# Performance work log

Hardware: AMD Instinct MI355X
Metric: run time of the kernel (lower is better)

Reference implementation:

```python
import jax, jax.numpy as jnp
import numpy as np

H = 800          # config.param.hidden_size (768 bert + 32 pos)
BERT_H = 768
POS_DIM = 32
NHEAD = 8
DH = 100         # gat_nhidden; NHEAD*DH == H
GAT_LAYERS = 2
N_EVENTS = 66
N_ROLES = 122
EPS = 0.1        # label smoothing
NEG_SLOPE = 0.2  # GATConv leaky_relu slope


def bilstm(x, Wih_f, Whh_f, b_f, Wih_b, Whh_b, b_b):
    """x: [B,T,D] -> [B,T,2H] (torch gate order i,f,g,o)."""
    def run(xs, Wih, Whh, b):
        B = xs.shape[1]; Hd = Whh.shape[1]
        def step(carry, xt):
            h, c = carry
            g = xt @ Wih.T + h @ Whh.T + b
            i, f, gg, o = jnp.split(g, 4, axis=-1)
            c = jax.nn.sigmoid(f) * c + jax.nn.sigmoid(i) * jnp.tanh(gg)
            h = jax.nn.sigmoid(o) * jnp.tanh(c)
            return (h, c), h
        init = (jnp.zeros((B, Hd), xs.dtype), jnp.zeros((B, Hd), xs.dtype))
        _, hs = jax.lax.scan(step, init, xs)
        return hs
    xt = jnp.swapaxes(x, 0, 1)                      # [T,B,D]
    hf = run(xt, Wih_f, Whh_f, b_f)
    hb = run(xt[::-1], Wih_b, Whh_b, b_b)[::-1]
    return jnp.swapaxes(jnp.concatenate([hf, hb], -1), 0, 1)


def gat_conv(x, src, dst, W, a_src, a_dst, bias):
    """PyG GATConv, concat heads, with self-loops. x:[n,H], src/dst:[E]."""
    n = x.shape[0]
    loops = jnp.arange(n)
    s = jnp.concatenate([src, loops])
    d = jnp.concatenate([dst, loops])
    h = (x @ W).reshape(n, NHEAD, DH)
    a_s = jnp.einsum('nhd,hd->nh', h, a_src)
    a_d = jnp.einsum('nhd,hd->nh', h, a_dst)
    e = jax.nn.leaky_relu(a_s[s] + a_d[d], NEG_SLOPE)              # [E,nh]
    m = jnp.full((n, NHEAD), -jnp.inf, x.dtype).at[d].max(e)       # segment max
    ex = jnp.exp(e - m[d])
    den = jnp.zeros((n, NHEAD), x.dtype).at[d].add(ex)
    alpha = ex / den[d]
    out = jnp.zeros((n, NHEAD, DH), x.dtype).at[d].add(alpha[..., None] * h[s])
    return out.reshape(n, NHEAD * DH) + bias


def label_smooth_ce(logits, target):
    c = logits.shape[-1]
    logp = jax.nn.log_softmax(logits, axis=-1)
    smooth = -logp.sum(-1)
    nll = -jnp.take_along_axis(logp, target[..., None], axis=-1)[..., 0]
    return smooth * EPS / c + (1.0 - EPS) * nll


def setup_inputs() -> dict:
    key = jax.random.key(0)
    ks = iter(jax.random.split(key, 32))
    B, S, E = 4, 128, 256
    std = 0.02
    inp = {}
    inp['bert_out'] = jax.random.normal(next(ks), (B, S + 1, BERT_H), jnp.float32)
    inp['pos_ids'] = jax.random.randint(next(ks), (B, S), 0, 31)
    inp['edge_src'] = jax.random.randint(next(ks), (B, E), 0, S)
    inp['edge_dst'] = jax.random.randint(next(ks), (B, E), 0, S)
    inp['start_labels'] = jax.random.randint(next(ks), (B, S, S), 0, N_EVENTS)
    inp['end_labels'] = jax.random.randint(next(ks), (B, S, S), 0, N_EVENTS)
    # parameters
    inp['pos_table'] = std * jax.random.normal(next(ks), (31, POS_DIM), jnp.float32)
    for sfx in ('f', 'b'):
        inp[f'Wih_{sfx}'] = std * jax.random.normal(next(ks), (4 * H, H), jnp.float32)
        inp[f'Whh_{sfx}'] = std * jax.random.normal(next(ks), (4 * H, H), jnp.float32)
        inp[f'bl_{sfx}'] = jnp.zeros((4 * H,), jnp.float32)
    inp['lstm_fc_W'] = std * jax.random.normal(next(ks), (2 * H, H), jnp.float32)
    inp['lstm_fc_b'] = jnp.zeros((H,), jnp.float32)
    inp['table_W'] = std * jax.random.normal(next(ks), (2 * H, H), jnp.float32)
    inp['table_b'] = jnp.zeros((H,), jnp.float32)
    inp['gat_W'] = std * jax.random.normal(next(ks), (H, NHEAD * DH), jnp.float32)
    inp['gat_asrc'] = std * jax.random.normal(next(ks), (NHEAD, DH), jnp.float32)
    inp['gat_adst'] = std * jax.random.normal(next(ks), (NHEAD, DH), jnp.float32)
    inp['gat_bias'] = jnp.zeros((NHEAD * DH,), jnp.float32)
    inp['trig_W'] = std * jax.random.normal(next(ks), (H, N_EVENTS), jnp.float32)
    inp['trig_b'] = jnp.zeros((N_EVENTS,), jnp.float32)
    inp['rs_W'] = std * jax.random.normal(next(ks), (H, N_ROLES), jnp.float32)
    inp['rs_b'] = jnp.zeros((N_ROLES,), jnp.float32)
    inp['re_W'] = std * jax.random.normal(next(ks), (H, N_ROLES), jnp.float32)
    inp['re_b'] = jnp.zeros((N_ROLES,), jnp.float32)
    return inp


def reference(bert_out, pos_ids, edge_src, edge_dst, start_labels, end_labels,
              pos_table, Wih_f, Whh_f, bl_f, Wih_b, Whh_b, bl_b,
              lstm_fc_W, lstm_fc_b, table_W, table_b,
              gat_W, gat_asrc, gat_adst, gat_bias,
              trig_W, trig_b, rs_W, rs_b, re_W, re_b):
    B, S = pos_ids.shape
    # POS embedding, prepend zero vector for [CLS] position
    pos_emb = pos_table[pos_ids]                                   # [B,S,32]
    pos_emb = jnp.concatenate(
        [jnp.zeros((B, 1, POS_DIM), bert_out.dtype), pos_emb], axis=1)
    x = jnp.concatenate([bert_out, pos_emb], axis=-1)              # [B,S+1,800]
    lstm_out = bilstm(x, Wih_f, Whh_f, bl_f, Wih_b, Whh_b, bl_b)   # [B,S+1,1600]
    x = x + jax.nn.relu(lstm_out @ lstm_fc_W + lstm_fc_b)
    x = x[:, 1:, :]                                                # drop CLS -> [B,S,800]

    # per-sample residual GAT stack (eval mode: dropout is identity)
    def gat_stack(xi, si, di):
        for _ in range(GAT_LAYERS):
            xi = xi + jax.nn.relu(gat_conv(xi, si, di, gat_W, gat_asrc, gat_adst, gat_bias))
        return xi
    x = jax.vmap(gat_stack)(x, edge_src, edge_dst)                 # [B,S,800]

    # pairwise table: cat(x_i, x_j) -> fc -> gelu
    x1 = jnp.broadcast_to(x[:, :, None, :], (B, S, S, H))
    x2 = jnp.broadcast_to(x[:, None, :, :], (B, S, S, H))
    s_tab = jax.nn.gelu(jnp.concatenate([x1, x2], -1) @ table_W + table_b)  # [B,S,S,800]

    eye = jnp.eye(S, dtype=start_labels.dtype)
    trig_mask = eye                                                # [S,S]
    arg_mask = 1 - eye
    trig_maskf = trig_mask.astype(s_tab.dtype)
    arg_maskf = arg_mask.astype(s_tab.dtype)

    trig_logits = s_tab @ trig_W + trig_b                          # [B,S,S,66]
    arg1_logits = s_tab @ rs_W + rs_b                              # [B,S,S,122]
    arg2_logits = s_tab @ re_W + re_b

    def masked_mean(loss, maskf):
        return (loss * maskf).sum((1, 2)) / maskf.sum()

    l1 = masked_mean(label_smooth_ce(trig_logits, start_labels * trig_mask), trig_maskf)
    l2 = masked_mean(label_smooth_ce(arg1_logits, start_labels * arg_mask), arg_maskf)
    l3 = masked_mean(label_smooth_ce(arg2_logits, end_labels * arg_mask), arg_maskf)
    total_loss = (l1 + l2 + l3).sum()

    trig_pred = jnp.argmax(trig_logits, -1)
    a1_pred = jnp.argmax(arg1_logits + jnp.swapaxes(arg1_logits, 1, 2), -1)
    a2_pred = jnp.argmax(arg2_logits + jnp.swapaxes(arg2_logits, 1, 2), -1)
    results1 = trig_pred * trig_mask + a1_pred * arg_mask
    results2 = trig_pred * trig_mask + a2_pred * arg_mask
    return total_loss, results1, results2
```

## Files before the change

kernel.cpp:

```cpp
#include <hip/hip_runtime.h>
#include <hip/hip_bf16.h>

#define B4 4
#define S128 128
#define T129 129
#define H800 800
#define E256 256
#define NE 66
#define NR 122
#define DPW 8
#define NWGD 100

typedef float f32x4 __attribute__((ext_vector_type(4)));

#define HB_ROW 900

__device__ __forceinline__ float gelu_f(float x) {
    float t = 0.7978845608028654f * (x + 0.044715f * x * x * x);
    float e = __expf(2.f * t);
    float th = 1.f - 2.f / (e + 1.f);
    return 0.5f * x * (1.f + th);
}

__device__ __forceinline__ float embed_at(const float* __restrict__ bert,
                                          const int* __restrict__ pids,
                                          const float* __restrict__ ptab,
                                          int m, int c)
{
    if (c < 768) return bert[(size_t)m * 768 + c];
    int t = m % T129, b = m / T129;
    if (t == 0) return 0.f;
    return ptab[pids[b * S128 + t - 1] * 32 + (c - 768)];
}

template<int AMODE, int BTRANS, int EPI>
__global__ __launch_bounds__(256) void k_gemm(const float* __restrict__ A, const float* __restrict__ Bm,
                                              const float* __restrict__ bias, const float* __restrict__ res,
                                              float* __restrict__ C, int M, int N, int K)
{
    __shared__ float As[16][68];
    __shared__ float Bs[16][68];
    int m0 = blockIdx.x * 64, n0 = blockIdx.y * 64;
    int tid = threadIdx.x;
    int tm = tid & 15, tn = tid >> 4;
    float acc[4][4] = {};
    for (int k0 = 0; k0 < K; k0 += 16) {
        {
            int kk = tid & 15, mmb = tid >> 4;
            #pragma unroll
            for (int q = 0; q < 4; q++) {
                int mm = mmb + q * 16;
                int m = m0 + mm;
                float v = 0.f;
                if (m < M) {
                    int row = (AMODE == 1) ? (m + (m >> 7) + 1) : m;
                    v = A[(size_t)row * K + k0 + kk];
                }
                As[kk][mm] = v;
            }
        }
        if (BTRANS == 0) {
            int nn = (tid & 15) * 4, kk2 = tid >> 4;
            int n = n0 + nn;
            float t0, t1, t2, t3;
            if (n + 3 < N) {
                const float4 bv = *(const float4*)&Bm[(size_t)(k0 + kk2) * N + n];
                t0 = bv.x; t1 = bv.y; t2 = bv.z; t3 = bv.w;
            } else {
                t0 = (n + 0 < N) ? Bm[(size_t)(k0 + kk2) * N + n + 0] : 0.f;
                t1 = (n + 1 < N) ? Bm[(size_t)(k0 + kk2) * N + n + 1] : 0.f;
                t2 = (n + 2 < N) ? Bm[(size_t)(k0 + kk2) * N + n + 2] : 0.f;
                t3 = (n + 3 < N) ? Bm[(size_t)(k0 + kk2) * N + n + 3] : 0.f;
            }
            Bs[kk2][nn + 0] = t0; Bs[kk2][nn + 1] = t1; Bs[kk2][nn + 2] = t2; Bs[kk2][nn + 3] = t3;
        } else {
            int kk = tid & 15, nnb = tid >> 4;
            #pragma unroll
            for (int q = 0; q < 4; q++) {
                int nn = nnb + q * 16;
                int n = n0 + nn;
                Bs[kk][nn] = (n < N) ? Bm[(size_t)n * K + k0 + kk] : 0.f;
            }
        }
        __syncthreads();
        #pragma unroll
        for (int kk = 0; kk < 16; kk++) {
            float4 a = *(const float4*)&As[kk][tm * 4];
            float4 bb = *(const float4*)&Bs[kk][tn * 4];
            float av[4] = {a.x, a.y, a.z, a.w};
            float bv[4] = {bb.x, bb.y, bb.z, bb.w};
            #pragma unroll
            for (int xx = 0; xx < 4; xx++)
                #pragma unroll
                for (int yy = 0; yy < 4; yy++)
                    acc[xx][yy] += av[xx] * bv[yy];
        }
        __syncthreads();
    }
    #pragma unroll
    for (int xx = 0; xx < 4; xx++) {
        int m = m0 + tm * 4 + xx;
        if (m >= M) continue;
        #pragma unroll
        for (int yy = 0; yy < 4; yy++) {
            int n = n0 + tn * 4 + yy;
            if (n >= N) continue;
            float v = acc[xx][yy];
            if (bias) v += bias[n];
            if (EPI == 1) v = res[(size_t)m * N + n] + fmaxf(v, 0.f);
            C[(size_t)m * N + n] = v;
        }
    }
}

__global__ __launch_bounds__(256) void k_gemm_wih(const float* __restrict__ bert,
                                                  const int* __restrict__ pids,
                                                  const float* __restrict__ ptab,
                                                  const float* __restrict__ Wf, const float* __restrict__ Wb,
                                                  const float* __restrict__ bf, const float* __restrict__ bb_,
                                                  float* __restrict__ C)
{
    __shared__ float As[16][68];
    __shared__ float Bs[16][68];
    const int M = 516, K = 800, N = 6400;
    int m0 = blockIdx.x * 64, n0 = blockIdx.y * 64;
    const float* W  = (n0 < 3200) ? Wf : Wb;
    const float* bi = (n0 < 3200) ? bf : bb_;
    int nb = (n0 < 3200) ? n0 : (n0 - 3200);
    int tid = threadIdx.x;
    int tm = tid & 15, tn = tid >> 4;
    int kk_s = tid & 15, mmb = tid >> 4;
    int mrow[4]; int pofs[4]; bool mok[4];
    #pragma unroll
    for (int q = 0; q < 4; q++) {
        int m = m0 + mmb + q * 16;
        mrow[q] = m;
        mok[q] = m < M;
        int t = m % T129, b = m / T129;
        pofs[q] = (mok[q] && t > 0) ? pids[b * S128 + t - 1] * 32 : -1;
    }
    float acc[4][4] = {};
    for (int k0 = 0; k0 < K; k0 += 16) {
        {
            int c = k0 + kk_s;
            #pragma unroll
            for (int q = 0; q < 4; q++) {
                float v = 0.f;
                if (mok[q]) {
                    if (c < 768) v = bert[(size_t)mrow[q] * 768 + c];
                    else         v = (pofs[q] < 0) ? 0.f : ptab[pofs[q] + c - 768];
                }
                As[kk_s][mmb + q * 16] = v;
            }
        }
        {
            int kk = tid & 15, nnb = tid >> 4;
            #pragma unroll
            for (int q = 0; q < 4; q++) {
                int nn = nnb + q * 16;
                Bs[kk][nn] = W[(size_t)(nb + nn) * K + k0 + kk];
            }
        }
        __syncthreads();
        #pragma unroll
        for (int kk = 0; kk < 16; kk++) {
            float4 a = *(const float4*)&As[kk][tm * 4];
            float4 bb = *(const float4*)&Bs[kk][tn * 4];
            float av[4] = {a.x, a.y, a.z, a.w};
            float bv[4] = {bb.x, bb.y, bb.z, bb.w};
            #pragma unroll
            for (int xx = 0; xx < 4; xx++)
                #pragma unroll
                for (int yy = 0; yy < 4; yy++)
                    acc[xx][yy] += av[xx] * bv[yy];
        }
        __syncthreads();
    }
    #pragma unroll
    for (int xx = 0; xx < 4; xx++) {
        int m = m0 + tm * 4 + xx;
        if (m >= M) continue;
        #pragma unroll
        for (int yy = 0; yy < 4; yy++) {
            int n = n0 + tn * 4 + yy;
            C[(size_t)m * N + n] = acc[xx][yy] + bi[nb + (n - n0)];
        }
    }
}

__global__ __launch_bounds__(256) void k_gemm_fc(const float* __restrict__ A, const float* __restrict__ Bm,
                                                 const float* __restrict__ bias,
                                                 const float* __restrict__ bert, const int* __restrict__ pids,
                                                 const float* __restrict__ ptab, float* __restrict__ C)
{
    __shared__ float As[16][68];
    __shared__ float Bs[16][68];
    const int M = 516, N = 800, K = 1600;
    int m0 = blockIdx.x * 64, n0 = blockIdx.y * 64;
    int tid = threadIdx.x;
    int tm = tid & 15, tn = tid >> 4;
    float acc[4][4] = {};
    for (int k0 = 0; k0 < K; k0 += 16) {
        {
            int kk = tid & 15, mmb = tid >> 4;
            #pragma unroll
            for (int q = 0; q < 4; q++) {
                int mm = mmb + q * 16;
                int m = m0 + mm;
                As[kk][mm] = (m < M) ? A[(size_t)m * K + k0 + kk] : 0.f;
            }
        }
        {
            int nn = (tid & 15) * 4, kk2 = tid >> 4;
            int n = n0 + nn;
            if (n + 3 < N) {
                *(float4*)&Bs[kk2][nn] = *(const float4*)&Bm[(size_t)(k0 + kk2) * N + n];
            } else {
                #pragma unroll
                for (int q = 0; q < 4; q++)
                    Bs[kk2][nn + q] = (n + q < N) ? Bm[(size_t)(k0 + kk2) * N + n + q] : 0.f;
            }
        }
        __syncthreads();
        #pragma unroll
        for (int kk = 0; kk < 16; kk++) {
            float4 a = *(const float4*)&As[kk][tm * 4];
            float4 bb = *(const float4*)&Bs[kk][tn * 4];
            float av[4] = {a.x, a.y, a.z, a.w};
            float bv[4] = {bb.x, bb.y, bb.z, bb.w};
            #pragma unroll
            for (int xx = 0; xx < 4; xx++)
                #pragma unroll
                for (int yy = 0; yy < 4; yy++)
                    acc[xx][yy] += av[xx] * bv[yy];
        }
        __syncthreads();
    }
    #pragma unroll
    for (int xx = 0; xx < 4; xx++) {
        int m = m0 + tm * 4 + xx;
        if (m >= M) continue;
        #pragma unroll
        for (int yy = 0; yy < 4; yy++) {
            int n = n0 + tn * 4 + yy;
            if (n >= N) continue;
            float v = fmaxf(acc[xx][yy] + bias[n], 0.f);
            C[(size_t)m * N + n] = embed_at(bert, pids, ptab, m, n) + v;
        }
    }
}

__global__ __launch_bounds__(256) void k_gemm_uv(const float* __restrict__ A, const float* __restrict__ tW,
                                                 const float* __restrict__ tb, float* __restrict__ C)
{
    __shared__ float As[16][68];
    __shared__ float Bs[16][68];
    const int M = 512, K = 800, N = 1600;
    int m0 = blockIdx.x * 64, n0 = blockIdx.y * 64;
    int tid = threadIdx.x;
    int tm = tid & 15, tn = tid >> 4;
    float acc[4][4] = {};
    for (int k0 = 0; k0 < K; k0 += 16) {
        {
            int kk = tid & 15, mmb = tid >> 4;
            #pragma unroll
            for (int q = 0; q < 4; q++) {
                int mm = mmb + q * 16;
                As[kk][mm] = A[(size_t)(m0 + mm) * K + k0 + kk];
            }
        }
        {
            int nn = (tid & 15) * 4, kk2 = tid >> 4;
            #pragma unroll
            for (int q = 0; q < 4; q++) {
                int n = n0 + nn + q;
                Bs[kk2][nn + q] = (n < 800) ? tW[(size_t)(k0 + kk2) * 800 + n]
                                            : tW[(size_t)(800 + k0 + kk2) * 800 + (n - 800)];
            }
        }
        __syncthreads();
        #pragma unroll
        for (int kk = 0; kk < 16; kk++) {
            float4 a = *(const float4*)&As[kk][tm * 4];
            float4 bb = *(const float4*)&Bs[kk][tn * 4];
            float av[4] = {a.x, a.y, a.z, a.w};
            float bv[4] = {bb.x, bb.y, bb.z, bb.w};
            #pragma unroll
            for (int xx = 0; xx < 4; xx++)
                #pragma unroll
                for (int yy = 0; yy < 4; yy++)
                    acc[xx][yy] += av[xx] * bv[yy];
        }
        __syncthreads();
    }
    #pragma unroll
    for (int xx = 0; xx < 4; xx++) {
        int m = m0 + tm * 4 + xx;
        #pragma unroll
        for (int yy = 0; yy < 4; yy++) {
            int n = n0 + tn * 4 + yy;
            float v = acc[xx][yy];
            if (n < 800) v += tb[n];
            C[(size_t)m * N + n] = v;
        }
    }
}

__global__ __launch_bounds__(256) void k_lstm(const float* __restrict__ xW,
                                              const float* __restrict__ Whhf, const float* __restrict__ Whhb,
                                              float* __restrict__ lstm, float* __restrict__ hpk)
{
    __shared__ float hb[4][HB_ROW];
    __shared__ float gsum[25][32][4];
    __shared__ float gg[128];
    int wg = blockIdx.x;
    int dir = wg >= NWGD ? 1 : 0;
    int wgd = dir ? wg - NWGD : wg;
    const float* Whh = dir ? Whhb : Whhf;
    const float* xWd = xW + dir * 3200;
    int tid = threadIdx.x;
    bool dotth = tid < 200;
    int d = tid & 7, sl = tid >> 3;
    int k0 = sl * 32;
    int rb = tid & 3, rd = (tid >> 2) & 7, rg = tid >> 5;
    int lane = tid & 63;

    float wreg[4][32];
    if (dotth) {
        #pragma unroll
        for (int g = 0; g < 4; g++) {
            const float* wp = Whh + (size_t)(g * 800 + wgd * DPW + d) * 800 + k0;
            #pragma unroll
            for (int q = 0; q < 32; q += 4)
                *(float4*)&wreg[g][q] = *(const float4*)&wp[q];
        }
    }
    for (int i = tid; i < 4 * HB_ROW; i += 256) (&hb[0][0])[i] = 0.f;
    __syncthreads();

    float cst = 0.f;

    for (int step = 0; step < 129; step++) {
        int t = dir ? (128 - step) : step;
        float xq = 0.f;
        if (tid < 128)
            xq = xWd[(size_t)(rb * T129 + t) * 6400 + rg * 800 + wgd * DPW + rd];
        if (step > 0) {
            int tprev = dir ? (t + 1) : (t - 1);
            if (tid < 200) {
                const f32x4* pb = (const f32x4*)(hpk + (size_t)(dir * 129 + tprev) * 3200);
                const f32x4* p0 = pb + tid;
                const f32x4* p1 = pb + tid + 200;
                const f32x4* p2 = pb + tid + 400;
                const f32x4* p3 = pb + tid + 600;
                f32x4 v0, v1, v2, v3;
                long long iters = 0;
                for (;;) {
                    asm volatile(
                        "global_load_dwordx4 %0, %4, off sc0 sc1\n\t"
                        "global_load_dwordx4 %1, %5, off sc0 sc1\n\t"
                        "global_load_dwordx4 %2, %6, off sc0 sc1\n\t"
                        "global_load_dwordx4 %3, %7, off sc0 sc1\n\t"
                        "s_waitcnt vmcnt(0)"
                        : "=&v"(v0), "=&v"(v1), "=&v"(v2), "=&v"(v3)
                        : "v"(p0), "v"(p1), "v"(p2), "v"(p3)
                        : "memory");
                    bool ok = fabsf(v0.x) < 1.5f && fabsf(v0.y) < 1.5f &&
                              fabsf(v0.z) < 1.5f && fabsf(v0.w) < 1.5f &&
                              fabsf(v1.x) < 1.5f && fabsf(v1.y) < 1.5f &&
                              fabsf(v1.z) < 1.5f && fabsf(v1.w) < 1.5f &&
                              fabsf(v2.x) < 1.5f && fabsf(v2.y) < 1.5f &&
                              fabsf(v2.z) < 1.5f && fabsf(v2.w) < 1.5f &&
                              fabsf(v3.x) < 1.5f && fabsf(v3.y) < 1.5f &&
                              fabsf(v3.z) < 1.5f && fabsf(v3.w) < 1.5f;
                    if (ok) break;
                    if (++iters > 20000000LL) break;
                }
                {
                    int s0 = tid;
                    int p_ = (s0 >> 3) * 8 + (s0 & 1) * 4;
                    ((f32x4*)&hb[0][0])[((s0 & 7) >> 1) * 225 + (p_ >> 5) * 9 + ((p_ & 31) >> 2)] = v0;
                }
                {
                    int s1 = tid + 200;
                    int p_ = (s1 >> 3) * 8 + (s1 & 1) * 4;
                    ((f32x4*)&hb[0][0])[((s1 & 7) >> 1) * 225 + (p_ >> 5) * 9 + ((p_ & 31) >> 2)] = v1;
                }
                {
                    int s2 = tid + 400;
                    int p_ = (s2 >> 3) * 8 + (s2 & 1) * 4;
                    ((f32x4*)&hb[0][0])[((s2 & 7) >> 1) * 225 + (p_ >> 5) * 9 + ((p_ & 31) >> 2)] = v2;
                }
                {
                    int s3 = tid + 600;
                    int p_ = (s3 >> 3) * 8 + (s3 & 1) * 4;
                    ((f32x4*)&hb[0][0])[((s3 & 7) >> 1) * 225 + (p_ >> 5) * 9 + ((p_ & 31) >> 2)] = v3;
                }
            }
            __syncthreads();
        }
        if (dotth) {
            float a[4][4] = {};
            #pragma unroll
            for (int b = 0; b < 4; b++) {
                const float* hrow = &hb[b][0];
                #pragma unroll
                for (int q = 0; q < 32; q += 4) {
                    float4 h = *(const float4*)&hrow[sl * 36 + q];
                    #pragma unroll
                    for (int g = 0; g < 4; g++)
                        a[g][b] += wreg[g][q] * h.x + wreg[g][q + 1] * h.y
                                 + wreg[g][q + 2] * h.z + wreg[g][q + 3] * h.w;
                }
            }
            #pragma unroll
            for (int g = 0; g < 4; g++)
                *(float4*)&gsum[sl][g * 8 + d][0] = make_float4(a[g][0], a[g][1], a[g][2], a[g][3]);
        }
        __syncthreads();
        if (tid < 128) {
            float s = xq;
            #pragma unroll
            for (int ss = 0; ss < 25; ss++) s += gsum[ss][rg * 8 + rd][rb];
            gg[tid] = s;
        }
        __syncthreads();
        float hv = 0.f;
        if (tid < 32) {
            int dd = tid & 7, bb2 = tid >> 3;
            float gi = gg[(0 << 5) | (dd << 2) | bb2];
            float gf = gg[(1 << 5) | (dd << 2) | bb2];
            float gG = gg[(2 << 5) | (dd << 2) | bb2];
            float go = gg[(3 << 5) | (dd << 2) | bb2];
            float si = 1.f / (1.f + __expf(-gi));
            float sf = 1.f / (1.f + __expf(-gf));
            float so = 1.f / (1.f + __expf(-go));
            cst = sf * cst + si * tanhf(gG);
            hv = so * tanhf(cst);
        }
        if (tid < 64) {
            int src = (lane & 7) * 4;
            f32x4 o;
            o.x = __shfl(hv, src + 0, 64);
            o.y = __shfl(hv, src + 1, 64);
            o.z = __shfl(hv, src + 2, 64);
            o.w = __shfl(hv, src + 3, 64);
            if (lane < 8) {
                float* pp = hpk + ((size_t)(dir * 129 + t) * 100 + wgd) * 32 + lane * 4;
                asm volatile("global_store_dwordx4 %0, %1, off sc0 sc1"
                             :: "v"((f32x4*)pp), "v"(o) : "memory");
            }
            if (lane < 8) {
                int bb = lane >> 1, half = lane & 1;
                float* ap = lstm + (size_t)((bb * T129 + t) * 1600) + dir * 800 + wgd * DPW + half * 4;
                asm volatile("global_store_dwordx4 %0, %1, off sc0 sc1"
                             :: "v"((f32x4*)ap), "v"(o) : "memory");
            }
        }
    }
}

template<int RESMODE>
__global__ __launch_bounds__(512) void k_gat_fused(const int* __restrict__ esrc, const int* __restrict__ edst,
                                                   const float* __restrict__ h1,
                                                   const float* __restrict__ asrc, const float* __restrict__ adst,
                                                   const float* __restrict__ gbias,
                                                   const float* __restrict__ res, float* __restrict__ out)
{
    __shared__ int se[384], de[384];
    __shared__ float asl[128], adl[128], ml[128], dl_[128];
    int bh = blockIdx.x;
    int b = bh >> 3, h = bh & 7;
    int t = threadIdx.x;
    if (t < 384) {
        if (t < E256) { se[t] = esrc[b * E256 + t]; de[t] = edst[b * E256 + t]; }
        else          { se[t] = t - E256;           de[t] = t - E256; }
    }
    int node = t >> 2, ch = t & 3;
    int dd0 = ch * 25;
    {
        const float* hp = h1 + (size_t)(b * S128 + node) * H800 + h * 100 + dd0;
        const float* ap = asrc + h * 100 + dd0;
        const float* dp = adst + h * 100 + dd0;
        float s1 = 0.f, s2 = 0.f;
        #pragma unroll
        for (int q = 0; q < 25; q++) { float hv = hp[q]; s1 += hv * ap[q]; s2 += hv * dp[q]; }
        s1 += __shfl_xor(s1, 1, 64); s1 += __shfl_xor(s1, 2, 64);
        s2 += __shfl_xor(s2, 1, 64); s2 += __shfl_xor(s2, 2, 64);
        if (ch == 0) { asl[node] = s1; adl[node] = s2; }
    }
    __syncthreads();
    if (t < 128) {
        float myad = adl[t];
        float m = -3.4e38f;
        for (int e = 0; e < 384; e++)
            if (de[e] == t) {
                float sc = asl[se[e]] + myad;
                sc = (sc > 0.f) ? sc : 0.2f * sc;
                m = fmaxf(m, sc);
            }
        float den = 0.f;
        for (int e = 0; e < 384; e++)
            if (de[e] == t) {
                float sc = asl[se[e]] + myad;
                sc = (sc > 0.f) ? sc : 0.2f * sc;
                den += __expf(sc - m);
            }
        ml[t] = m; dl_[t] = den;
    }
    __syncthreads();
    float acc[25] = {};
    float myad = adl[node], mym = ml[node];
    for (int e = 0; e < 384; e++) {
        if (de[e] == node) {
            int s = se[e];
            float sc = asl[s] + myad;
            sc = (sc > 0.f) ? sc : 0.2f * sc;
            float w = __expf(sc - mym);
            const float* hp = h1 + (size_t)(b * S128 + s) * H800 + h * 100 + dd0;
            #pragma unroll
            for (int q = 0; q < 25; q++) acc[q] += w * hp[q];
        }
    }
    float inv = 1.f / dl_[node];
    int n = b * S128 + node;
    size_t rrow = (RESMODE == 1) ? (size_t)(n + b + 1) * H800 : (size_t)n * H800;
    #pragma unroll
    for (int q = 0; q < 25; q++) {
        int col = h * 100 + dd0 + q;
        float v = acc[q] * inv + gbias[col];
        out[(size_t)n * H800 + col] = res[rrow + col] + fmaxf(v, 0.f);
    }
}

__global__ __launch_bounds__(64) void k_trig(const float* __restrict__ uv,
                                             const float* __restrict__ W, const float* __restrict__ bias,
                                             const int* __restrict__ labels, float* __restrict__ d_out)
{
    __shared__ float s[800];
    __shared__ float lg[66];
    int bi = blockIdx.x;
    int i = bi & 127;
    int l = threadIdx.x;
    const float* ur = uv + (size_t)bi * 1600;
    const float* vr = ur + 800;
    for (int k = l; k < 800; k += 64) s[k] = gelu_f(ur[k] + vr[k]);
    __syncthreads();
    float a0 = 0.f, a1 = 0.f;
    bool has2 = (l < 2);
    for (int k = 0; k < 800; k++) {
        float sv = s[k];
        a0 += sv * W[k * NE + l];
        if (has2) a1 += sv * W[k * NE + 64 + l];
    }
    lg[l] = a0 + bias[l];
    if (has2) lg[64 + l] = a1 + bias[64 + l];
    __syncthreads();
    if (l == 0) {
        float m = lg[0];
        for (int c = 1; c < NE; c++) m = fmaxf(m, lg[c]);
        float se = 0.f, sl = 0.f, bv = lg[0];
        int am = 0;
        for (int c = 0; c < NE; c++) {
            se += __expf(lg[c] - m);
            sl += lg[c];
            if (lg[c] > bv) { bv = lg[c]; am = c; }
        }
        float lse = m + __logf(se);
        int tgt = labels[(size_t)bi * S128 + i];
        float ce = (0.1f / NE) * (NE * lse - sl) + 0.9f * (lse - lg[tgt]);
        atomicAdd(d_out, ce * (1.f / 128.f));
        int r = bi * S128 + i;
        d_out[1 + r] = (float)am;
        d_out[1 + 65536 + r] = (float)am;
    }
}

__global__ __launch_bounds__(256) void k_logits2(const float* __restrict__ uvb,
                                                 const float* __restrict__ rsW, const float* __restrict__ rsb,
                                                 const float* __restrict__ reW, const float* __restrict__ reb,
                                                 float* __restrict__ L)
{
    __shared__ float As[16][68];
    __shared__ float Bs[16][256];
    int bi = blockIdx.y;
    const float* base = uvb + (size_t)bi * 128 * 1600;
    float* Lb = L + (size_t)bi * 16384 * 256;
    int il = blockIdx.x >> 1;
    int j0 = (blockIdx.x & 1) * 64;
    const float* urow = base + (size_t)il * 1600;
    int tid = threadIdx.x;
    int tm = tid & 7, tn = tid >> 3;
    float acc[8][8] = {};
    int ct = tid;
    int hc = (ct < 128) ? ct : (ct - 128);
    const float* Wp = (ct < 128) ? rsW : reW;
    bool cok = hc < NR;
    for (int k0 = 0; k0 < 800; k0 += 16) {
        {
            int kk = tid & 15, rrb = tid >> 4;
            float uk = urow[k0 + kk];
            #pragma unroll
            for (int q = 0; q < 4; q++) {
                int rr = rrb + q * 16;
                float xv = uk + base[(size_t)(j0 + rr) * 1600 + 800 + k0 + kk];
                As[kk][rr] = gelu_f(xv);
            }
        }
        #pragma unroll
        for (int kk2 = 0; kk2 < 16; kk2++)
            Bs[kk2][ct] = cok ? Wp[(size_t)(k0 + kk2) * NR + hc] : 0.f;
        __syncthreads();
        #pragma unroll
        for (int kk = 0; kk < 16; kk++) {
            float4 a0 = *(const float4*)&As[kk][tm * 8];
            float4 a1 = *(const float4*)&As[kk][tm * 8 + 4];
            float4 b0 = *(const float4*)&Bs[kk][tn * 8];
            float4 b1 = *(const float4*)&Bs[kk][tn * 8 + 4];
            float av[8] = {a0.x, a0.y, a0.z, a0.w, a1.x, a1.y, a1.z, a1.w};
            float bv[8] = {b0.x, b0.y, b0.z, b0.w, b1.x, b1.y, b1.z, b1.w};
            #pragma unroll
            for (int xx = 0; xx < 8; xx++)
                #pragma unroll
                for (int yy = 0; yy < 8; yy++)
                    acc[xx][yy] += av[xx] * bv[yy];
        }
        __syncthreads();
    }
    int head = tn >> 4;
    const float* bp = head ? reb : rsb;
    #pragma unroll
    for (int xx = 0; xx < 8; xx++) {
        int r = il * S128 + j0 + tm * 8 + xx;
        float* Lr = Lb + (size_t)r * 256 + tn * 8;
        #pragma unroll
        for (int hf = 0; hf < 2; hf++) {
            int c = (tn * 8 + hf * 4) & 127;
            if (c + 3 < NR) {
                float4 o = make_float4(acc[xx][hf*4+0] + bp[c+0], acc[xx][hf*4+1] + bp[c+1],
                                       acc[xx][hf*4+2] + bp[c+2], acc[xx][hf*4+3] + bp[c+3]);
                *(float4*)(Lr + hf * 4) = o;
            } else {
                #pragma unroll
                for (int q = 0; q < 4; q++)
                    if (c + q < NR) Lr[hf * 4 + q] = acc[xx][hf*4+q] + bp[c+q];
            }
        }
    }
}

__global__ __launch_bounds__(256) void k_loss2(const float* __restrict__ L,
                                               const int* __restrict__ lab0, const int* __restrict__ lab1,
                                               float* __restrict__ res0, float* __restrict__ res1,
                                               float* __restrict__ lossptr)
{
    __shared__ float wsum[4];
    int wv = threadIdx.x >> 6, l = threadIdx.x & 63;
    int rr = blockIdx.x * 4 + wv;
    int bi = rr >> 14;
    int r = rr & 16383;
    int i = r >> 7, j = r & 127;
    size_t bioff = (size_t)bi * 16384;
    float ces = 0.f;
    if (i != j) {
        const float* row  = L + (bioff + r) * 256;
        const float* prow = L + (bioff + ((j << 7) | i)) * 256;
        bool v2 = (l < NR - 64);
        #pragma unroll
        for (int hd = 0; hd < 2; hd++) {
            const float* rw = row + hd * 128;
            const float* pw = prow + hd * 128;
            float x1 = rw[l];
            float x2 = v2 ? rw[l + 64] : -3.4e38f;
            float m = fmaxf(x1, x2);
            #pragma unroll
            for (int s = 32; s; s >>= 1) m = fmaxf(m, __shfl_xor(m, s, 64));
            float se = __expf(x1 - m) + (v2 ? __expf(x2 - m) : 0.f);
            float sl = x1 + (v2 ? x2 : 0.f);
            #pragma unroll
            for (int s = 32; s; s >>= 1) { se += __shfl_xor(se, s, 64); sl += __shfl_xor(sl, s, 64); }
            float lse = m + __logf(se);
            int tgt = (hd ? lab1 : lab0)[bioff + r];
            float lt = rw[tgt];
            ces += (0.1f / NR) * (NR * lse - sl) + 0.9f * (lse - lt);
            float y1 = x1 + pw[l];
            float y2 = v2 ? (x2 + pw[l + 64]) : -3.4e38f;
            float bv; int bidx;
            if (y2 > y1) { bv = y2; bidx = l + 64; } else { bv = y1; bidx = l; }
            #pragma unroll
            for (int s = 32; s; s >>= 1) {
                float ov = __shfl_xor(bv, s, 64);
                int oi = __shfl_xor(bidx, s, 64);
                if (ov > bv || (ov == bv && oi < bidx)) { bv = ov; bidx = oi; }
            }
            if (l == 0) (hd ? res1 : res0)[bioff + r] = (float)bidx;
        }
    }
    if (l == 0) wsum[wv] = ces;
    __syncthreads();
    if (threadIdx.x == 0) {
        float s = (wsum[0] + wsum[1] + wsum[2] + wsum[3]) * (1.f / 16256.f);
        atomicAdd(lossptr, s);
    }
}

extern "C" void kernel_launch(void* const* d_in, const int* in_sizes, int n_in,
                              void* d_out, int out_size, void* d_ws, size_t ws_size,
                              hipStream_t stream)
{
    (void)in_sizes; (void)n_in; (void)out_size; (void)ws_size;
    const float* bert  = (const float*)d_in[0];
    const int*   pids  = (const int*)d_in[1];
    const int*   esrc  = (const int*)d_in[2];
    const int*   edst  = (const int*)d_in[3];
    const int*   slab  = (const int*)d_in[4];
    const int*   elab  = (const int*)d_in[5];
    const float* ptab  = (const float*)d_in[6];
    const float* Wih_f = (const float*)d_in[7];
    const float* Whh_f = (const float*)d_in[8];
    const float* bl_f  = (const float*)d_in[9];
    const float* Wih_b = (const float*)d_in[10];
    const float* Whh_b = (const float*)d_in[11];
    const float* bl_b  = (const float*)d_in[12];
    const float* fcW   = (const float*)d_in[13];
    const float* fcb   = (const float*)d_in[14];
    const float* tW    = (const float*)d_in[15];
    const float* tb    = (const float*)d_in[16];
    const float* gatW  = (const float*)d_in[17];
    const float* asrc  = (const float*)d_in[18];
    const float* adst  = (const float*)d_in[19];
    const float* gbias = (const float*)d_in[20];
    const float* trigW = (const float*)d_in[21];
    const float* trigb = (const float*)d_in[22];
    const float* rsW   = (const float*)d_in[23];
    const float* rsb   = (const float*)d_in[24];
    const float* reW   = (const float*)d_in[25];
    const float* reb   = (const float*)d_in[26];
    float* out = (float*)d_out;

    float* ws = (float*)d_ws;
    size_t off = 0;
    auto alloc = [&](size_t n) { float* p = ws + off; off += (n + 255) & ~(size_t)255; return p; };
    float* uv    = alloc((size_t)512 * 1600);
    float* R     = ws + off;
    size_t roff = 0;
    auto ralloc = [&](size_t n) { float* p = R + roff; roff += (n + 255) & ~(size_t)255; return p; };
    float* xW   = ralloc((size_t)516 * 6400);
    float* lstm = ralloc((size_t)516 * 1600);
    float* xg   = ralloc(516 * 800);
    float* h1   = ralloc(512 * 800);
    float* g1   = ralloc(512 * 800);
    float* g2   = ralloc(512 * 800);
    float* hpk  = ralloc((size_t)2 * 129 * 100 * 32);
    float* Lbuf = R;

    hipMemsetAsync(d_out, 0, 4, stream);
    hipMemsetAsync(hpk, 0x7F, (size_t)2 * 129 * 100 * 32 * sizeof(float), stream);

    k_gemm_wih<<<dim3(9, 100), 256, 0, stream>>>(bert, pids, ptab, Wih_f, Wih_b, bl_f, bl_b, xW);

    k_lstm<<<2 * NWGD, 256, 0, stream>>>(xW, Whh_f, Whh_b, lstm, hpk);

    k_gemm_fc<<<dim3(9, 13), 256, 0, stream>>>(lstm, fcW, fcb, bert, pids, ptab, xg);

    k_gemm<1, 0, 0><<<dim3(8, 13), 256, 0, stream>>>(xg, gatW, nullptr, nullptr, h1, 512, 800, 800);
    k_gat_fused<1><<<32, 512, 0, stream>>>(esrc, edst, h1, asrc, adst, gbias, xg, g1);
    k_gemm<0, 0, 0><<<dim3(8, 13), 256, 0, stream>>>(g1, gatW, nullptr, nullptr, h1, 512, 800, 800);
    k_gat_fused<0><<<32, 512, 0, stream>>>(esrc, edst, h1, asrc, adst, gbias, g1, g2);

    k_gemm_uv<<<dim3(8, 25), 256, 0, stream>>>(g2, tW, tb, uv);

    k_trig<<<512, 64, 0, stream>>>(uv, trigW, trigb, slab, out);

    for (int bp = 0; bp < 2; bp++) {
        k_logits2<<<dim3(256, 2), 256, 0, stream>>>(uv + (size_t)bp * 2 * 128 * 1600,
                                                    rsW, rsb, reW, reb, Lbuf);
        k_loss2<<<8192, 256, 0, stream>>>(Lbuf,
                                          slab + (size_t)bp * 2 * 16384, elab + (size_t)bp * 2 * 16384,
                                          out + 1 + (size_t)bp * 2 * 16384,
                                          out + 1 + 65536 + (size_t)bp * 2 * 16384, out);
    }
}
```

Baseline: 2.190 ms.

## Poll LSTM step flags with one wave and fuse gate reduction via shuffles

Each recurrent step now has a single wavefront spin on one sentinel float per producer workgroup slot, followed by a block barrier. Only after that does the full 200-thread load of the previous hidden state run, which cuts the volume of coherent polling traffic. The gate-sum reduction and LSTM cell update are merged into one 64-thread pass. Each lane handles two batches, and gate values are exchanged with shuffles instead of a shared gg buffer, which drops one __syncthreads per step. The extra barrier after polling and the retained full-load check add some latency in exchange.

```diff
diff --git a/kernel.cpp b/kernel.cpp
--- a/kernel.cpp
+++ b/kernel.cpp
@@ -312,7 +312,6 @@
 {
     __shared__ float hb[4][HB_ROW];
     __shared__ float gsum[25][32][4];
-    __shared__ float gg[128];
     int wg = blockIdx.x;
     int dir = wg >= NWGD ? 1 : 0;
     int wgd = dir ? wg - NWGD : wg;
@@ -322,8 +321,8 @@
     bool dotth = tid < 200;
     int d = tid & 7, sl = tid >> 3;
     int k0 = sl * 32;
-    int rb = tid & 3, rd = (tid >> 2) & 7, rg = tid >> 5;
     int lane = tid & 63;
+    int rg = lane & 3, rd2 = (lane >> 2) & 7, rbase = lane >> 5;
 
     float wreg[4][32];
     if (dotth) {
@@ -338,17 +337,43 @@
     for (int i = tid; i < 4 * HB_ROW; i += 256) (&hb[0][0])[i] = 0.f;
     __syncthreads();
 
-    float cst = 0.f;
+    float cst0 = 0.f, cst1 = 0.f;
 
     for (int step = 0; step < 129; step++) {
         int t = dir ? (128 - step) : step;
-        float xq = 0.f;
-        if (tid < 128)
-            xq = xWd[(size_t)(rb * T129 + t) * 6400 + rg * 800 + wgd * DPW + rd];
+        float xq0 = 0.f, xq1 = 0.f;
+        if (tid < 64) {
+            size_t col = (size_t)rg * 800 + wgd * DPW + rd2;
+            xq0 = xWd[(size_t)((rbase    ) * T129 + t) * 6400 + col];
+            xq1 = xWd[(size_t)((rbase + 2) * T129 + t) * 6400 + col];
+        }
         if (step > 0) {
             int tprev = dir ? (t + 1) : (t - 1);
+            const float* rowb = hpk + (size_t)(dir * 129 + tprev) * 3200;
+            if (tid < 64) {
+                bool mine = lane < 50;
+                const float* q0 = rowb + (size_t)(lane * 2 + 0) * 32;
+                const float* q1 = rowb + (size_t)(lane * 2 + 1) * 32;
+                long long iters = 0;
+                for (;;) {
+                    float f0 = 0.f, f1 = 0.f;
+                    if (mine) {
+                        asm volatile(
+                            "global_load_dword %0, %2, off sc0 sc1\n\t"
+                            "global_load_dword %1, %3, off sc0 sc1\n\t"
+                            "s_waitcnt vmcnt(0)"
+                            : "=&v"(f0), "=&v"(f1)
+                            : "v"(q0), "v"(q1)
+                            : "memory");
+                    }
+                    bool ok = !mine || (fabsf(f0) < 1.5f && fabsf(f1) < 1.5f);
+                    if (__all(ok)) break;
+                    if (++iters > 20000000LL) break;
+                }
+            }
+            __syncthreads();
             if (tid < 200) {
-                const f32x4* pb = (const f32x4*)(hpk + (size_t)(dir * 129 + tprev) * 3200);
+                const f32x4* pb = (const f32x4*)rowb;
                 const f32x4* p0 = pb + tid;
                 const f32x4* p1 = pb + tid + 200;
                 const f32x4* p2 = pb + tid + 400;
@@ -418,41 +443,49 @@
                 *(float4*)&gsum[sl][g * 8 + d][0] = make_float4(a[g][0], a[g][1], a[g][2], a[g][3]);
         }
         __syncthreads();
-        if (tid < 128) {
-            float s = xq;
-            #pragma unroll
-            for (int ss = 0; ss < 25; ss++) s += gsum[ss][rg * 8 + rd][rb];
-            gg[tid] = s;
-        }
-        __syncthreads();
-        float hv = 0.f;
-        if (tid < 32) {
-            int dd = tid & 7, bb2 = tid >> 3;
-            float gi = gg[(0 << 5) | (dd << 2) | bb2];
-            float gf = gg[(1 << 5) | (dd << 2) | bb2];
-            float gG = gg[(2 << 5) | (dd << 2) | bb2];
-            float go = gg[(3 << 5) | (dd << 2) | bb2];
-            float si = 1.f / (1.f + __expf(-gi));
-            float sf = 1.f / (1.f + __expf(-gf));
-            float so = 1.f / (1.f + __expf(-go));
-            cst = sf * cst + si * tanhf(gG);
-            hv = so * tanhf(cst);
-        }
         if (tid < 64) {
-            int src = (lane & 7) * 4;
+            float s0 = xq0, s1 = xq1;
+            int gi_ = rg * 8 + rd2;
+            #pragma unroll
+            for (int ss = 0; ss < 25; ss++) {
+                s0 += gsum[ss][gi_][rbase];
+                s1 += gsum[ss][gi_][rbase + 2];
+            }
+            int base = lane & ~3;
+            float gi0 = __shfl(s0, base + 0, 64);
+            float gf0 = __shfl(s0, base + 1, 64);
+            float gG0 = __shfl(s0, base + 2, 64);
+            float go0 = __shfl(s0, base + 3, 64);
+            float gi1 = __shfl(s1, base + 0, 64);
+            float gf1 = __shfl(s1, base + 1, 64);
+            float gG1 = __shfl(s1, base + 2, 64);
+            float go1 = __shfl(s1, base + 3, 64);
+            float si0 = 1.f / (1.f + __expf(-gi0));
+            float sf0 = 1.f / (1.f + __expf(-gf0));
+            float so0 = 1.f / (1.f + __expf(-go0));
+            cst0 = sf0 * cst0 + si0 * tanhf(gG0);
+            float hv0 = so0 * tanhf(cst0);
+            float si1 = 1.f / (1.f + __expf(-gi1));
+            float sf1 = 1.f / (1.f + __expf(-gf1));
+            float so1 = 1.f / (1.f + __expf(-go1));
+            cst1 = sf1 * cst1 + si1 * tanhf(cst1 * 0.f + gG1);
+            hv0 = hv0;
+            float hv1 = so1 * tanhf(cst1);
+            int bb = lane >> 1, d0 = (lane & 1) * 4;
             f32x4 o;
-            o.x = __shfl(hv, src + 0, 64);
-            o.y = __shfl(hv, src + 1, 64);
-            o.z = __shfl(hv, src + 2, 64);
-            o.w = __shfl(hv, src + 3, 64);
+            #pragma unroll
+            for (int j = 0; j < 4; j++) {
+                int srcl = ((bb & 1) << 5) + (d0 + j) * 4;
+                float a0 = __shfl(hv0, srcl, 64);
+                float a1 = __shfl(hv1, srcl, 64);
+                o[j] = (bb >= 2) ? a1 : a0;
+            }
             if (lane < 8) {
                 float* pp = hpk + ((size_t)(dir * 129 + t) * 100 + wgd) * 32 + lane * 4;
                 asm volatile("global_store_dwordx4 %0, %1, off sc0 sc1"
                              :: "v"((f32x4*)pp), "v"(o) : "memory");
-            }
-            if (lane < 8) {
-                int bb = lane >> 1, half = lane & 1;
-                float* ap = lstm + (size_t)((bb * T129 + t) * 1600) + dir * 800 + wgd * DPW + half * 4;
+                int bb2 = lane >> 1, half = lane & 1;
+                float* ap = lstm + (size_t)((bb2 * T129 + t) * 1600) + dir * 800 + wgd * DPW + half * 4;
                 asm volatile("global_store_dwordx4 %0, %1, off sc0 sc1"
                              :: "v"((f32x4*)ap), "v"(o) : "memory");
             }
```

After: 2.270 ms. +3.7%, slower.
